# Optimization experiments

Measured on AMD Instinct MI355X. Metric: run time of the kernel, lower is better.

## Reference

```python
import jax, jax.numpy as jnp
import numpy as np

B, S, D, H, DFF = 2, 2048, 768, 12, 3072
DH = D // H
EPS = 1e-5


def _ln(x, g, b):
    m = jnp.mean(x, axis=-1, keepdims=True)
    v = jnp.mean((x - m) ** 2, axis=-1, keepdims=True)
    return (x - m) * jax.lax.rsqrt(v + EPS) * g + b


def setup_inputs() -> dict:
    key = jax.random.key(0)
    ks = jax.random.split(key, 13)
    sd = 1.0 / np.sqrt(D)
    sf = 1.0 / np.sqrt(DFF)
    return {
        "x": jax.random.normal(ks[0], (B, S, D), jnp.float32),
        "Wq": jax.random.uniform(ks[1], (D, D), jnp.float32, -sd, sd),
        "bq": jnp.zeros((D,), jnp.float32),
        "Wk": jax.random.uniform(ks[2], (D, D), jnp.float32, -sd, sd),
        "bk": jnp.zeros((D,), jnp.float32),
        "Wv": jax.random.uniform(ks[3], (D, D), jnp.float32, -sd, sd),
        "bv": jnp.zeros((D,), jnp.float32),
        "Wo": jax.random.uniform(ks[4], (D, D), jnp.float32, -sd, sd),
        "bo": jnp.zeros((D,), jnp.float32),
        "W1": jax.random.uniform(ks[5], (D, DFF), jnp.float32, -sd, sd),
        "b1": jnp.zeros((DFF,), jnp.float32),
        "W2": jax.random.uniform(ks[6], (DFF, D), jnp.float32, -sf, sf),
        "b2": jnp.zeros((D,), jnp.float32),
        "g1": jnp.ones((D,), jnp.float32),
        "be1": jnp.zeros((D,), jnp.float32),
        "g2": jnp.ones((D,), jnp.float32),
        "be2": jnp.zeros((D,), jnp.float32),
    }


def reference(x, Wq, bq, Wk, bk, Wv, bv, Wo, bo, W1, b1, W2, b2, g1, be1, g2, be2):
    # QKV projections, then split heads: [B,S,D] -> [B,H,S,DH]
    def heads(t):
        return t.reshape(B, S, H, DH).transpose(0, 2, 1, 3)
    Q = heads(x @ Wq + bq)
    K = heads(x @ Wk + bk)
    V = heads(x @ Wv + bv)
    # Per-head loop in original == batched-over-heads attention here (same math)
    scores = jnp.einsum("bhqd,bhkd->bhqk", Q, K) / np.sqrt(DH)
    attn = jax.nn.softmax(scores, axis=-1)  # [B,H,S,S] -- dominant intermediate
    ctx = jnp.einsum("bhqk,bhkd->bhqd", attn, V)
    ctx = ctx.transpose(0, 2, 1, 3).reshape(B, S, D)  # concat heads
    x = x + (ctx @ Wo + bo)
    x = _ln(x, g1, be1)
    ffn = (jax.nn.gelu(x @ W1 + b1, approximate=False)) @ W2 + b2
    x = _ln(x + ffn, g2, be2)
    return x
```

## Files before the change

kernel.cpp:

```cpp
#include <hip/hip_runtime.h>
#include <math.h>

#define BB 2
#define SS 2048
#define DD 768
#define HH 12
#define DHH 64
#define DFFN 3072
#define MTOK (BB*SS)

typedef __attribute__((ext_vector_type(8))) __bf16 bf16x8;
typedef __attribute__((ext_vector_type(4))) float f32x4;
typedef __attribute__((ext_vector_type(16))) float f32x16;

__device__ __forceinline__ unsigned short f2bf(float f) {
    unsigned int b = __builtin_bit_cast(unsigned int, f);
    b += 0x7FFFu + ((b >> 16) & 1u);
    return (unsigned short)(b >> 16);
}

__device__ __forceinline__ void gload_lds16(const void* g, void* l) {
    __builtin_amdgcn_global_load_lds((const __attribute__((address_space(1))) unsigned int*)g,
                                     (__attribute__((address_space(3))) unsigned int*)l,
                                     16, 0, 0);
}

template <int ACT, int OBF>
__global__ __launch_bounds__(256) void gemm_mfma(const unsigned short* __restrict__ A,
                                                 const unsigned short* __restrict__ Bt,
                                                 const float* __restrict__ bias,
                                                 void* __restrict__ Cout,
                                                 int M, int N, int ldA, int ldB, int Klen) {
    __shared__ unsigned short As[128 * 64];
    __shared__ unsigned short Bs[128 * 64];
    const int tid = threadIdx.x;
    const int lane = tid & 63;
    const int w = tid >> 6;
    const int l15 = lane & 15, l4 = lane >> 4;
    const int m0 = blockIdx.x * 128;
    const int n0 = blockIdx.y * 128;
    const int wr = (w >> 1) * 64;
    const int wc = (w & 1) * 64;

    f32x4 acc[4][4] = {};

    int srow[4], scd[4];
#pragma unroll
    for (int i = 0; i < 4; ++i) {
        int s = w * 256 + i * 64 + lane;
        srow[i] = s >> 3;
        scd[i] = (((s & 7) ^ (srow[i] & 7))) * 8;
    }

    for (int k0 = 0; k0 < Klen; k0 += 64) {
        __syncthreads();
#pragma unroll
        for (int i = 0; i < 4; ++i) {
            const unsigned short* gA = A + (size_t)(m0 + srow[i]) * ldA + k0 + scd[i];
            gload_lds16(gA, &As[(w * 256 + i * 64) * 8]);
        }
#pragma unroll
        for (int i = 0; i < 4; ++i) {
            const unsigned short* gB = Bt + (size_t)(n0 + srow[i]) * ldB + k0 + scd[i];
            gload_lds16(gB, &Bs[(w * 256 + i * 64) * 8]);
        }
        __syncthreads();
#pragma unroll
        for (int ks = 0; ks < 2; ++ks) {
            bf16x8 af[4], bfr[4];
#pragma unroll
            for (int m = 0; m < 4; ++m) {
                int r = wr + m * 16 + l15;
                int c = (ks * 4 + l4) ^ (r & 7);
                af[m] = *(const bf16x8*)&As[(r * 8 + c) * 8];
            }
#pragma unroll
            for (int n = 0; n < 4; ++n) {
                int r = wc + n * 16 + l15;
                int c = (ks * 4 + l4) ^ (r & 7);
                bfr[n] = *(const bf16x8*)&Bs[(r * 8 + c) * 8];
            }
#pragma unroll
            for (int m = 0; m < 4; ++m)
#pragma unroll
                for (int n = 0; n < 4; ++n)
                    acc[m][n] = __builtin_amdgcn_mfma_f32_16x16x32_bf16(af[m], bfr[n], acc[m][n], 0, 0, 0);
        }
    }

#pragma unroll
    for (int n = 0; n < 4; ++n) {
        int col = n0 + wc + n * 16 + l15;
        float bv = bias ? bias[col] : 0.0f;
#pragma unroll
        for (int m = 0; m < 4; ++m) {
#pragma unroll
            for (int r = 0; r < 4; ++r) {
                int row = m0 + wr + m * 16 + l4 * 4 + r;
                float v = acc[m][n][r] + bv;
                if (ACT) v = 0.5f * v * (1.0f + erff(v * 0.70710678118654752f));
                if (OBF) ((unsigned short*)Cout)[(size_t)row * N + col] = f2bf(v);
                else     ((float*)Cout)[(size_t)row * N + col] = v;
            }
        }
    }
}

__global__ __launch_bounds__(256) void attn_mfma2(const unsigned short* __restrict__ QKV,
                                                  const unsigned short* __restrict__ Vt,
                                                  unsigned short* __restrict__ Ctx) {
    __shared__ unsigned short Ks[64 * 64];
    __shared__ unsigned short Vs[64 * 64];
    const int tid = threadIdx.x;
    const int lane = tid & 63;
    const int w = tid >> 6;
    const int l31 = lane & 31;
    const int hi = lane >> 5;
    const int bh = blockIdx.y;
    const int b = bh / HH, h = bh % HH;
    const int q0 = blockIdx.x * 128 + w * 32;
    const float CLOG = 0.18033688011112042f;

    bf16x8 qf[4];
    {
        const unsigned short* qp = QKV + (size_t)(b * SS + q0 + l31) * 2304 + h * 64 + hi * 8;
        qf[0] = *(const bf16x8*)qp;
        qf[1] = *(const bf16x8*)(qp + 16);
        qf[2] = *(const bf16x8*)(qp + 32);
        qf[3] = *(const bf16x8*)(qp + 48);
    }

    f32x16 oacc[2] = {};
    float m_run = -1e30f, l_run = 0.0f;

    int arow[2], acd[2];
#pragma unroll
    for (int i = 0; i < 2; ++i) {
        int s = w * 128 + i * 64 + lane;
        arow[i] = s >> 3;
        acd[i] = ((s & 7) ^ (arow[i] & 7)) * 8;
    }

    for (int kt = 0; kt < SS / 64; ++kt) {
        const int k0 = kt * 64;
        __syncthreads();
#pragma unroll
        for (int i = 0; i < 2; ++i) {
            const unsigned short* gK = QKV + (size_t)(b * SS + k0 + arow[i]) * 2304 + DD + h * 64 + acd[i];
            gload_lds16(gK, &Ks[(w * 128 + i * 64) * 8]);
        }
#pragma unroll
        for (int i = 0; i < 2; ++i) {
            const unsigned short* gV = Vt + (size_t)(bh * 64 + arow[i]) * SS + k0 + acd[i];
            gload_lds16(gV, &Vs[(w * 128 + i * 64) * 8]);
        }
        __syncthreads();

        f32x16 st[2] = {};
#pragma unroll
        for (int t = 0; t < 2; ++t) {
#pragma unroll
            for (int ks = 0; ks < 4; ++ks) {
                int row = 32 * t + l31;
                int ch = (2 * ks + hi) ^ (row & 7);
                bf16x8 kf = *(const bf16x8*)&Ks[(row * 8 + ch) * 8];
                st[t] = __builtin_amdgcn_mfma_f32_32x32x16_bf16(kf, qf[ks], st[t], 0, 0, 0);
            }
        }

        float pmax = st[0][0];
#pragma unroll
        for (int r = 1; r < 16; ++r) pmax = fmaxf(pmax, st[0][r]);
#pragma unroll
        for (int r = 0; r < 16; ++r) pmax = fmaxf(pmax, st[1][r]);
        pmax = fmaxf(pmax, __shfl_xor(pmax, 32));
        pmax *= CLOG;
        const float mn = fmaxf(m_run, pmax);
        const float corr = exp2f(m_run - mn);

        unsigned int Wn[2][4][2];
        float rs = 0.0f;
#pragma unroll
        for (int t = 0; t < 2; ++t) {
#pragma unroll
            for (int blk = 0; blk < 4; ++blk) {
                float pa = exp2f(fmaf(st[t][4 * blk + 0], CLOG, -mn));
                float pb = exp2f(fmaf(st[t][4 * blk + 1], CLOG, -mn));
                float pc = exp2f(fmaf(st[t][4 * blk + 2], CLOG, -mn));
                float pd = exp2f(fmaf(st[t][4 * blk + 3], CLOG, -mn));
                rs += (pa + pb) + (pc + pd);
                Wn[t][blk][0] = (unsigned int)f2bf(pa) | ((unsigned int)f2bf(pb) << 16);
                Wn[t][blk][1] = (unsigned int)f2bf(pc) | ((unsigned int)f2bf(pd) << 16);
            }
        }
        rs += __shfl_xor(rs, 32);
        l_run = l_run * corr + rs;
        m_run = mn;

#pragma unroll
        for (int d = 0; d < 2; ++d)
#pragma unroll
            for (int r = 0; r < 16; ++r) oacc[d][r] *= corr;

        unsigned int PW[2][4][2];
#pragma unroll
        for (int t = 0; t < 2; ++t)
#pragma unroll
            for (int blk = 0; blk < 4; ++blk)
#pragma unroll
                for (int u = 0; u < 2; ++u) PW[t][blk][u] = __shfl_xor(Wn[t][blk][u], 32);

        const bool h1 = (hi == 1);
#pragma unroll
        for (int t = 0; t < 2; ++t) {
#pragma unroll
            for (int ks2 = 0; ks2 < 2; ++ks2) {
                union { unsigned int u[4]; bf16x8 v; } pu;
                pu.u[0] = h1 ? PW[t][2 * ks2 + 1][0] : Wn[t][2 * ks2][0];
                pu.u[1] = h1 ? PW[t][2 * ks2 + 1][1] : Wn[t][2 * ks2][1];
                pu.u[2] = h1 ? Wn[t][2 * ks2 + 1][0] : PW[t][2 * ks2][0];
                pu.u[3] = h1 ? Wn[t][2 * ks2 + 1][1] : PW[t][2 * ks2][1];
#pragma unroll
                for (int d = 0; d < 2; ++d) {
                    int row = 32 * d + l31;
                    int ch = (4 * t + 2 * ks2 + hi) ^ (row & 7);
                    bf16x8 vf = *(const bf16x8*)&Vs[(row * 8 + ch) * 8];
                    oacc[d] = __builtin_amdgcn_mfma_f32_32x32x16_bf16(vf, pu.v, oacc[d], 0, 0, 0);
                }
            }
        }
    }

    const float inv = 1.0f / l_run;
    unsigned short* cp = Ctx + (size_t)(b * SS + q0 + l31) * DD + h * 64;
#pragma unroll
    for (int d = 0; d < 2; ++d) {
#pragma unroll
        for (int blk = 0; blk < 4; ++blk) {
            unsigned long long pk =
                  (unsigned long long)f2bf(oacc[d][4 * blk + 0] * inv)
                | ((unsigned long long)f2bf(oacc[d][4 * blk + 1] * inv) << 16)
                | ((unsigned long long)f2bf(oacc[d][4 * blk + 2] * inv) << 32)
                | ((unsigned long long)f2bf(oacc[d][4 * blk + 3] * inv) << 48);
            *(unsigned long long*)(cp + 32 * d + 8 * blk + 4 * hi) = pk;
        }
    }
}

__global__ __launch_bounds__(256) void v_transpose(const unsigned short* __restrict__ QKV,
                                                   unsigned short* __restrict__ Vt) {
    __shared__ unsigned short t[64][66];
    const int tid = threadIdx.x;
    const int bh = blockIdx.y, b = bh / HH, h = bh % HH;
    const int s0 = blockIdx.x * 64;
    const int c = tid & 63, r0 = tid >> 6;
#pragma unroll
    for (int i = 0; i < 16; ++i) {
        int r = i * 4 + r0;
        t[r][c] = QKV[(size_t)(b * SS + s0 + r) * 2304 + 1536 + h * 64 + c];
    }
    __syncthreads();
#pragma unroll
    for (int i = 0; i < 16; ++i) {
        int r = i * 4 + r0;
        Vt[((size_t)bh * 64 + r) * SS + s0 + c] = t[c][r];
    }
}

__global__ __launch_bounds__(256) void wtrans(const float* __restrict__ W,
                                              unsigned short* __restrict__ Wt,
                                              int K, int N, int rowoff) {
    __shared__ float t[32][33];
    const int tid = threadIdx.x;
    const int k0 = blockIdx.x * 32, n0 = blockIdx.y * 32;
    const int c = tid & 31, r0 = tid >> 5;
#pragma unroll
    for (int i = 0; i < 4; ++i) {
        int r = i * 8 + r0;
        t[r][c] = W[(size_t)(k0 + r) * N + n0 + c];
    }
    __syncthreads();
#pragma unroll
    for (int i = 0; i < 4; ++i) {
        int r = i * 8 + r0;
        Wt[(size_t)(rowoff + n0 + r) * K + k0 + c] = f2bf(t[c][r]);
    }
}

__global__ __launch_bounds__(256) void f2b_vec(const float* __restrict__ in,
                                               unsigned short* __restrict__ out, int n4) {
    int i = blockIdx.x * 256 + threadIdx.x;
    if (i < n4) {
        float4 v = ((const float4*)in)[i];
        unsigned long long pk = (unsigned long long)f2bf(v.x)
                              | ((unsigned long long)f2bf(v.y) << 16)
                              | ((unsigned long long)f2bf(v.z) << 32)
                              | ((unsigned long long)f2bf(v.w) << 48);
        ((unsigned long long*)out)[i] = pk;
    }
}

__global__ __launch_bounds__(256) void bias_concat(const float* __restrict__ q,
                                                   const float* __restrict__ k,
                                                   const float* __restrict__ v,
                                                   float* __restrict__ o) {
    int i = blockIdx.x * 256 + threadIdx.x;
    if (i < DD) { o[i] = q[i]; o[DD + i] = k[i]; o[2 * DD + i] = v[i]; }
}

template <int WB>
__global__ __launch_bounds__(256) void add_ln3(const float* __restrict__ a,
                                               const float* __restrict__ p1,
                                               const float* __restrict__ p2,
                                               const float* __restrict__ bias,
                                               const float* __restrict__ g,
                                               const float* __restrict__ be,
                                               float* __restrict__ outf,
                                               unsigned short* __restrict__ outb) {
    const int row = blockIdx.x;
    const int tid = threadIdx.x;
    float x[3];
    float s = 0.0f, s2 = 0.0f;
#pragma unroll
    for (int i = 0; i < 3; ++i) {
        int c = tid + i * 256;
        size_t idx = (size_t)row * DD + c;
        float v = a[idx] + p1[idx] + p2[idx] + bias[c];
        x[i] = v; s += v; s2 += v * v;
    }
#pragma unroll
    for (int off = 32; off; off >>= 1) {
        s += __shfl_down(s, off);
        s2 += __shfl_down(s2, off);
    }
    __shared__ float ws[8];
    const int wid = tid >> 6, lane = tid & 63;
    if (lane == 0) { ws[wid] = s; ws[4 + wid] = s2; }
    __syncthreads();
    if (tid == 0) {
        ws[0] = ws[0] + ws[1] + ws[2] + ws[3];
        ws[4] = ws[4] + ws[5] + ws[6] + ws[7];
    }
    __syncthreads();
    const float mean = ws[0] * (1.0f / DD);
    const float var = ws[4] * (1.0f / DD) - mean * mean;
    const float inv = rsqrtf(var + 1e-5f);
#pragma unroll
    for (int i = 0; i < 3; ++i) {
        int c = tid + i * 256;
        float res = (x[i] - mean) * inv * g[c] + be[c];
        outf[(size_t)row * DD + c] = res;
        if (WB) outb[(size_t)row * DD + c] = f2bf(res);
    }
}

extern "C" void kernel_launch(void* const* d_in, const int* in_sizes, int n_in,
                              void* d_out, int out_size, void* d_ws, size_t ws_size,
                              hipStream_t stream) {
    const float* x   = (const float*)d_in[0];
    const float* Wq  = (const float*)d_in[1];
    const float* bq  = (const float*)d_in[2];
    const float* Wk  = (const float*)d_in[3];
    const float* bk  = (const float*)d_in[4];
    const float* Wv  = (const float*)d_in[5];
    const float* bv  = (const float*)d_in[6];
    const float* Wo  = (const float*)d_in[7];
    const float* bo  = (const float*)d_in[8];
    const float* W1  = (const float*)d_in[9];
    const float* b1  = (const float*)d_in[10];
    const float* W2  = (const float*)d_in[11];
    const float* b2  = (const float*)d_in[12];
    const float* g1  = (const float*)d_in[13];
    const float* be1 = (const float*)d_in[14];
    const float* g2  = (const float*)d_in[15];
    const float* be2 = (const float*)d_in[16];
    float* out = (float*)d_out;

    char* w8 = (char*)d_ws;
    unsigned short* QKV = (unsigned short*)w8;
    unsigned short* Hff = (unsigned short*)w8;
    unsigned short* Vt  = (unsigned short*)(w8 + 18874368);
    unsigned short* Ctxb  = (unsigned short*)(w8 + 25165824);
    unsigned short* xb    = (unsigned short*)(w8 + 31457280);
    unsigned short* Wqkvt = (unsigned short*)(w8 + 37748736);
    unsigned short* Wot   = (unsigned short*)(w8 + 41287680);
    unsigned short* W1t   = (unsigned short*)(w8 + 42467328);
    unsigned short* W2t   = (unsigned short*)(w8 + 47185920);
    float* bqkv = (float*)(w8 + 51904512);
    float* Pa   = (float*)(w8 + 51916800);
    float* Pb   = (float*)(w8 + 64499712);
    float* X2   = (float*)(w8 + 77082624);

    dim3 blk(256);

    f2b_vec<<<dim3(3072), blk, 0, stream>>>(x, xb, MTOK * DD / 4);
    wtrans<<<dim3(24, 24), blk, 0, stream>>>(Wq, Wqkvt, DD, DD, 0);
    wtrans<<<dim3(24, 24), blk, 0, stream>>>(Wk, Wqkvt, DD, DD, DD);
    wtrans<<<dim3(24, 24), blk, 0, stream>>>(Wv, Wqkvt, DD, DD, 2 * DD);
    wtrans<<<dim3(24, 24), blk, 0, stream>>>(Wo, Wot, DD, DD, 0);
    wtrans<<<dim3(24, 96), blk, 0, stream>>>(W1, W1t, DD, DFFN, 0);
    wtrans<<<dim3(96, 24), blk, 0, stream>>>(W2, W2t, DFFN, DD, 0);
    bias_concat<<<dim3(3), blk, 0, stream>>>(bq, bk, bv, bqkv);

    gemm_mfma<0, 1><<<dim3(32, 18), blk, 0, stream>>>(xb, Wqkvt, bqkv, QKV,
                                                      MTOK, 3 * DD, DD, DD, DD);
    v_transpose<<<dim3(32, 24), blk, 0, stream>>>(QKV, Vt);
    attn_mfma2<<<dim3(SS / 128, BB * HH), blk, 0, stream>>>(QKV, Vt, Ctxb);
    gemm_mfma<0, 0><<<dim3(32, 6), blk, 0, stream>>>(Ctxb, Wot, nullptr, Pa,
                                                     MTOK, DD, DD, DD, 384);
    gemm_mfma<0, 0><<<dim3(32, 6), blk, 0, stream>>>(Ctxb + 384, Wot + 384, nullptr, Pb,
                                                     MTOK, DD, DD, DD, 384);
    add_ln3<1><<<dim3(MTOK), blk, 0, stream>>>(x, Pa, Pb, bo, g1, be1, X2, xb);
    gemm_mfma<1, 1><<<dim3(32, 24), blk, 0, stream>>>(xb, W1t, b1, Hff,
                                                      MTOK, DFFN, DD, DD, DD);
    gemm_mfma<0, 0><<<dim3(32, 6), blk, 0, stream>>>(Hff, W2t, nullptr, Pa,
                                                     MTOK, DD, DFFN, DFFN, 1536);
    gemm_mfma<0, 0><<<dim3(32, 6), blk, 0, stream>>>(Hff + 1536, W2t + 1536, nullptr, Pb,
                                                     MTOK, DD, DFFN, DFFN, 1536);
    add_ln3<0><<<dim3(MTOK), blk, 0, stream>>>(X2, Pa, Pb, b2, g2, be2, out, nullptr);
}
```

Before: 387.2 us.

## Double-buffer GEMM/attention tiles, split attention KV in two, lazy softmax rescale

Adds double-buffered LDS prefetch to the GEMM and attention kernels so global loads overlap MFMA work. Attention is split across two KV halves via grid z, writing unnormalized float partials plus max/sum, merged by a new combine kernel. Online softmax skips rescaling unless the max grows by more than a threshold. Split-K GEMMs now use grid z instead of two launches. This adds partial-output traffic and an extra launch, and doubles LDS use per block.

```diff
diff --git a/kernel.cpp b/kernel.cpp
--- a/kernel.cpp
+++ b/kernel.cpp
@@ -31,16 +31,20 @@
                                                  const float* __restrict__ bias,
                                                  void* __restrict__ Cout,
                                                  int M, int N, int ldA, int ldB, int Klen) {
-    __shared__ unsigned short As[128 * 64];
-    __shared__ unsigned short Bs[128 * 64];
+    __shared__ unsigned short As[2 * 128 * 64];
+    __shared__ unsigned short Bs[2 * 128 * 64];
     const int tid = threadIdx.x;
     const int lane = tid & 63;
     const int w = tid >> 6;
     const int l15 = lane & 15, l4 = lane >> 4;
     const int m0 = blockIdx.x * 128;
     const int n0 = blockIdx.y * 128;
+    const int z = blockIdx.z;
     const int wr = (w >> 1) * 64;
     const int wc = (w & 1) * 64;
+
+    const unsigned short* Az = A + (size_t)z * Klen;
+    const unsigned short* Bz = Bt + (size_t)z * Klen;
 
     f32x4 acc[4][4] = {};
 
@@ -52,19 +56,27 @@
         scd[i] = (((s & 7) ^ (srow[i] & 7))) * 8;
     }
 
+#pragma unroll
+    for (int i = 0; i < 4; ++i) {
+        gload_lds16(Az + (size_t)(m0 + srow[i]) * ldA + scd[i], &As[(w * 256 + i * 64) * 8]);
+        gload_lds16(Bz + (size_t)(n0 + srow[i]) * ldB + scd[i], &Bs[(w * 256 + i * 64) * 8]);
+    }
+    __syncthreads();
+
+    int cb = 0;
     for (int k0 = 0; k0 < Klen; k0 += 64) {
-        __syncthreads();
-#pragma unroll
-        for (int i = 0; i < 4; ++i) {
-            const unsigned short* gA = A + (size_t)(m0 + srow[i]) * ldA + k0 + scd[i];
-            gload_lds16(gA, &As[(w * 256 + i * 64) * 8]);
-        }
-#pragma unroll
-        for (int i = 0; i < 4; ++i) {
-            const unsigned short* gB = Bt + (size_t)(n0 + srow[i]) * ldB + k0 + scd[i];
-            gload_lds16(gB, &Bs[(w * 256 + i * 64) * 8]);
-        }
-        __syncthreads();
+        if (k0 + 64 < Klen) {
+            const int nb = (cb ^ 1) * 128 * 64;
+#pragma unroll
+            for (int i = 0; i < 4; ++i) {
+                gload_lds16(Az + (size_t)(m0 + srow[i]) * ldA + k0 + 64 + scd[i],
+                            &As[nb + (w * 256 + i * 64) * 8]);
+                gload_lds16(Bz + (size_t)(n0 + srow[i]) * ldB + k0 + 64 + scd[i],
+                            &Bs[nb + (w * 256 + i * 64) * 8]);
+            }
+        }
+        const unsigned short* Ac = &As[cb * 128 * 64];
+        const unsigned short* Bc = &Bs[cb * 128 * 64];
 #pragma unroll
         for (int ks = 0; ks < 2; ++ks) {
             bf16x8 af[4], bfr[4];
@@ -72,13 +84,13 @@
             for (int m = 0; m < 4; ++m) {
                 int r = wr + m * 16 + l15;
                 int c = (ks * 4 + l4) ^ (r & 7);
-                af[m] = *(const bf16x8*)&As[(r * 8 + c) * 8];
+                af[m] = *(const bf16x8*)&Ac[(r * 8 + c) * 8];
             }
 #pragma unroll
             for (int n = 0; n < 4; ++n) {
                 int r = wc + n * 16 + l15;
                 int c = (ks * 4 + l4) ^ (r & 7);
-                bfr[n] = *(const bf16x8*)&Bs[(r * 8 + c) * 8];
+                bfr[n] = *(const bf16x8*)&Bc[(r * 8 + c) * 8];
             }
 #pragma unroll
             for (int m = 0; m < 4; ++m)
@@ -86,8 +98,11 @@
                 for (int n = 0; n < 4; ++n)
                     acc[m][n] = __builtin_amdgcn_mfma_f32_16x16x32_bf16(af[m], bfr[n], acc[m][n], 0, 0, 0);
         }
-    }
-
+        __syncthreads();
+        cb ^= 1;
+    }
+
+    const size_t zoff = (size_t)z * M * N;
 #pragma unroll
     for (int n = 0; n < 4; ++n) {
         int col = n0 + wc + n * 16 + l15;
@@ -100,17 +115,18 @@
                 float v = acc[m][n][r] + bv;
                 if (ACT) v = 0.5f * v * (1.0f + erff(v * 0.70710678118654752f));
                 if (OBF) ((unsigned short*)Cout)[(size_t)row * N + col] = f2bf(v);
-                else     ((float*)Cout)[(size_t)row * N + col] = v;
-            }
-        }
-    }
-}
-
-__global__ __launch_bounds__(256) void attn_mfma2(const unsigned short* __restrict__ QKV,
+                else     ((float*)Cout)[zoff + (size_t)row * N + col] = v;
+            }
+        }
+    }
+}
+
+__global__ __launch_bounds__(256) void attn_mfma3(const unsigned short* __restrict__ QKV,
                                                   const unsigned short* __restrict__ Vt,
-                                                  unsigned short* __restrict__ Ctx) {
-    __shared__ unsigned short Ks[64 * 64];
-    __shared__ unsigned short Vs[64 * 64];
+                                                  float* __restrict__ Opart,
+                                                  float* __restrict__ ML) {
+    __shared__ unsigned short Ks[2 * 64 * 64];
+    __shared__ unsigned short Vs[2 * 64 * 64];
     const int tid = threadIdx.x;
     const int lane = tid & 63;
     const int w = tid >> 6;
@@ -118,6 +134,7 @@
     const int hi = lane >> 5;
     const int bh = blockIdx.y;
     const int b = bh / HH, h = bh % HH;
+    const int z = blockIdx.z;
     const int q0 = blockIdx.x * 128 + w * 32;
     const float CLOG = 0.18033688011112042f;
 
@@ -141,20 +158,31 @@
         acd[i] = ((s & 7) ^ (arow[i] & 7)) * 8;
     }
 
-    for (int kt = 0; kt < SS / 64; ++kt) {
-        const int k0 = kt * 64;
-        __syncthreads();
-#pragma unroll
-        for (int i = 0; i < 2; ++i) {
-            const unsigned short* gK = QKV + (size_t)(b * SS + k0 + arow[i]) * 2304 + DD + h * 64 + acd[i];
-            gload_lds16(gK, &Ks[(w * 128 + i * 64) * 8]);
-        }
-#pragma unroll
-        for (int i = 0; i < 2; ++i) {
-            const unsigned short* gV = Vt + (size_t)(bh * 64 + arow[i]) * SS + k0 + acd[i];
-            gload_lds16(gV, &Vs[(w * 128 + i * 64) * 8]);
-        }
-        __syncthreads();
+    const int kbase = z * (SS / 2);
+#pragma unroll
+    for (int i = 0; i < 2; ++i) {
+        gload_lds16(QKV + (size_t)(b * SS + kbase + arow[i]) * 2304 + DD + h * 64 + acd[i],
+                    &Ks[(w * 128 + i * 64) * 8]);
+        gload_lds16(Vt + (size_t)(bh * 64 + arow[i]) * SS + kbase + acd[i],
+                    &Vs[(w * 128 + i * 64) * 8]);
+    }
+    __syncthreads();
+
+    int cb = 0;
+    for (int it = 0; it < SS / 128; ++it) {
+        if (it + 1 < SS / 128) {
+            const int k0n = kbase + (it + 1) * 64;
+            const int nb = (cb ^ 1) * 64 * 64;
+#pragma unroll
+            for (int i = 0; i < 2; ++i) {
+                gload_lds16(QKV + (size_t)(b * SS + k0n + arow[i]) * 2304 + DD + h * 64 + acd[i],
+                            &Ks[nb + (w * 128 + i * 64) * 8]);
+                gload_lds16(Vt + (size_t)(bh * 64 + arow[i]) * SS + k0n + acd[i],
+                            &Vs[nb + (w * 128 + i * 64) * 8]);
+            }
+        }
+        const unsigned short* Kc = &Ks[cb * 64 * 64];
+        const unsigned short* Vc = &Vs[cb * 64 * 64];
 
         f32x16 st[2] = {};
 #pragma unroll
@@ -163,7 +191,7 @@
             for (int ks = 0; ks < 4; ++ks) {
                 int row = 32 * t + l31;
                 int ch = (2 * ks + hi) ^ (row & 7);
-                bf16x8 kf = *(const bf16x8*)&Ks[(row * 8 + ch) * 8];
+                bf16x8 kf = *(const bf16x8*)&Kc[(row * 8 + ch) * 8];
                 st[t] = __builtin_amdgcn_mfma_f32_32x32x16_bf16(kf, qf[ks], st[t], 0, 0, 0);
             }
         }
@@ -175,8 +203,17 @@
         for (int r = 0; r < 16; ++r) pmax = fmaxf(pmax, st[1][r]);
         pmax = fmaxf(pmax, __shfl_xor(pmax, 32));
         pmax *= CLOG;
-        const float mn = fmaxf(m_run, pmax);
-        const float corr = exp2f(m_run - mn);
+
+        if (!__all(pmax <= m_run + 8.0f)) {
+            float mn = fmaxf(m_run, pmax);
+            float corr = exp2f(m_run - mn);
+#pragma unroll
+            for (int d = 0; d < 2; ++d)
+#pragma unroll
+                for (int r = 0; r < 16; ++r) oacc[d][r] *= corr;
+            l_run *= corr;
+            m_run = mn;
+        }
 
         unsigned int Wn[2][4][2];
         float rs = 0.0f;
@@ -184,66 +221,80 @@
         for (int t = 0; t < 2; ++t) {
 #pragma unroll
             for (int blk = 0; blk < 4; ++blk) {
-                float pa = exp2f(fmaf(st[t][4 * blk + 0], CLOG, -mn));
-                float pb = exp2f(fmaf(st[t][4 * blk + 1], CLOG, -mn));
-                float pc = exp2f(fmaf(st[t][4 * blk + 2], CLOG, -mn));
-                float pd = exp2f(fmaf(st[t][4 * blk + 3], CLOG, -mn));
+                float pa = exp2f(fmaf(st[t][4 * blk + 0], CLOG, -m_run));
+                float pb = exp2f(fmaf(st[t][4 * blk + 1], CLOG, -m_run));
+                float pc = exp2f(fmaf(st[t][4 * blk + 2], CLOG, -m_run));
+                float pd = exp2f(fmaf(st[t][4 * blk + 3], CLOG, -m_run));
                 rs += (pa + pb) + (pc + pd);
                 Wn[t][blk][0] = (unsigned int)f2bf(pa) | ((unsigned int)f2bf(pb) << 16);
                 Wn[t][blk][1] = (unsigned int)f2bf(pc) | ((unsigned int)f2bf(pd) << 16);
             }
         }
         rs += __shfl_xor(rs, 32);
-        l_run = l_run * corr + rs;
-        m_run = mn;
-
-#pragma unroll
-        for (int d = 0; d < 2; ++d)
-#pragma unroll
-            for (int r = 0; r < 16; ++r) oacc[d][r] *= corr;
-
-        unsigned int PW[2][4][2];
-#pragma unroll
-        for (int t = 0; t < 2; ++t)
-#pragma unroll
-            for (int blk = 0; blk < 4; ++blk)
-#pragma unroll
-                for (int u = 0; u < 2; ++u) PW[t][blk][u] = __shfl_xor(Wn[t][blk][u], 32);
-
-        const bool h1 = (hi == 1);
+        l_run += rs;
+
 #pragma unroll
         for (int t = 0; t < 2; ++t) {
 #pragma unroll
             for (int ks2 = 0; ks2 < 2; ++ks2) {
+                unsigned int ex0 = __shfl_xor(hi ? Wn[t][2 * ks2][0] : Wn[t][2 * ks2 + 1][0], 32);
+                unsigned int ex1 = __shfl_xor(hi ? Wn[t][2 * ks2][1] : Wn[t][2 * ks2 + 1][1], 32);
                 union { unsigned int u[4]; bf16x8 v; } pu;
-                pu.u[0] = h1 ? PW[t][2 * ks2 + 1][0] : Wn[t][2 * ks2][0];
-                pu.u[1] = h1 ? PW[t][2 * ks2 + 1][1] : Wn[t][2 * ks2][1];
-                pu.u[2] = h1 ? Wn[t][2 * ks2 + 1][0] : PW[t][2 * ks2][0];
-                pu.u[3] = h1 ? Wn[t][2 * ks2 + 1][1] : PW[t][2 * ks2][1];
+                pu.u[0] = hi ? ex0 : Wn[t][2 * ks2][0];
+                pu.u[1] = hi ? ex1 : Wn[t][2 * ks2][1];
+                pu.u[2] = hi ? Wn[t][2 * ks2 + 1][0] : ex0;
+                pu.u[3] = hi ? Wn[t][2 * ks2 + 1][1] : ex1;
 #pragma unroll
                 for (int d = 0; d < 2; ++d) {
                     int row = 32 * d + l31;
                     int ch = (4 * t + 2 * ks2 + hi) ^ (row & 7);
-                    bf16x8 vf = *(const bf16x8*)&Vs[(row * 8 + ch) * 8];
+                    bf16x8 vf = *(const bf16x8*)&Vc[(row * 8 + ch) * 8];
                     oacc[d] = __builtin_amdgcn_mfma_f32_32x32x16_bf16(vf, pu.v, oacc[d], 0, 0, 0);
                 }
             }
         }
-    }
-
-    const float inv = 1.0f / l_run;
-    unsigned short* cp = Ctx + (size_t)(b * SS + q0 + l31) * DD + h * 64;
+        __syncthreads();
+        cb ^= 1;
+    }
+
+    float* op = Opart + (size_t)z * MTOK * DD + (size_t)(b * SS + q0 + l31) * DD + h * 64;
 #pragma unroll
     for (int d = 0; d < 2; ++d) {
 #pragma unroll
         for (int blk = 0; blk < 4; ++blk) {
-            unsigned long long pk =
-                  (unsigned long long)f2bf(oacc[d][4 * blk + 0] * inv)
-                | ((unsigned long long)f2bf(oacc[d][4 * blk + 1] * inv) << 16)
-                | ((unsigned long long)f2bf(oacc[d][4 * blk + 2] * inv) << 32)
-                | ((unsigned long long)f2bf(oacc[d][4 * blk + 3] * inv) << 48);
-            *(unsigned long long*)(cp + 32 * d + 8 * blk + 4 * hi) = pk;
-        }
+            float4 v = make_float4(oacc[d][4 * blk + 0], oacc[d][4 * blk + 1],
+                                   oacc[d][4 * blk + 2], oacc[d][4 * blk + 3]);
+            *(float4*)(op + 32 * d + 8 * blk + 4 * hi) = v;
+        }
+    }
+    if (hi == 0) {
+        size_t mi = (((size_t)z * BB * HH + bh) * SS + (q0 + l31)) * 2;
+        ML[mi] = m_run;
+        ML[mi + 1] = l_run;
+    }
+}
+
+__global__ __launch_bounds__(256) void attn_combine(const float* __restrict__ Opart,
+                                                    const float* __restrict__ ML,
+                                                    unsigned short* __restrict__ Ctx) {
+    const int row = blockIdx.x;
+    const int tid = threadIdx.x;
+    const int b = row >> 11, s = row & 2047;
+    const float* r0 = Opart + (size_t)row * DD;
+    const float* r1 = Opart + (size_t)MTOK * DD + (size_t)row * DD;
+    unsigned short* co = Ctx + (size_t)row * DD;
+#pragma unroll
+    for (int i = 0; i < 3; ++i) {
+        int c = tid + i * 256;
+        int h = c >> 6;
+        size_t i0 = (((size_t)(b * HH + h)) * SS + s) * 2;
+        size_t i1 = (((size_t)(BB * HH + b * HH + h)) * SS + s) * 2;
+        float m0 = ML[i0], l0 = ML[i0 + 1];
+        float m1 = ML[i1], l1 = ML[i1 + 1];
+        float M = fmaxf(m0, m1);
+        float w0 = exp2f(m0 - M), w1 = exp2f(m1 - M);
+        float inv = 1.0f / (w0 * l0 + w1 * l1);
+        co[c] = f2bf((r0[c] * w0 + r1[c] * w1) * inv);
     }
 }
 
@@ -390,6 +441,7 @@
     float* Pa   = (float*)(w8 + 51916800);
     float* Pb   = (float*)(w8 + 64499712);
     float* X2   = (float*)(w8 + 77082624);
+    float* ML   = (float*)(w8 + 89665536);
 
     dim3 blk(256);
 
@@ -402,20 +454,17 @@
     wtrans<<<dim3(96, 24), blk, 0, stream>>>(W2, W2t, DFFN, DD, 0);
     bias_concat<<<dim3(3), blk, 0, stream>>>(bq, bk, bv, bqkv);
 
-    gemm_mfma<0, 1><<<dim3(32, 18), blk, 0, stream>>>(xb, Wqkvt, bqkv, QKV,
-                                                      MTOK, 3 * DD, DD, DD, DD);
+    gemm_mfma<0, 1><<<dim3(32, 18, 1), blk, 0, stream>>>(xb, Wqkvt, bqkv, QKV,
+                                                         MTOK, 3 * DD, DD, DD, DD);
     v_transpose<<<dim3(32, 24), blk, 0, stream>>>(QKV, Vt);
-    attn_mfma2<<<dim3(SS / 128, BB * HH), blk, 0, stream>>>(QKV, Vt, Ctxb);
-    gemm_mfma<0, 0><<<dim3(32, 6), blk, 0, stream>>>(Ctxb, Wot, nullptr, Pa,
-                                                     MTOK, DD, DD, DD, 384);
-    gemm_mfma<0, 0><<<dim3(32, 6), blk, 0, stream>>>(Ctxb + 384, Wot + 384, nullptr, Pb,
-                                                     MTOK, DD, DD, DD, 384);
+    attn_mfma3<<<dim3(SS / 128, BB * HH, 2), blk, 0, stream>>>(QKV, Vt, Pa, ML);
+    attn_combine<<<dim3(MTOK), blk, 0, stream>>>(Pa, ML, Ctxb);
+    gemm_mfma<0, 0><<<dim3(32, 6, 2), blk, 0, stream>>>(Ctxb, Wot, nullptr, Pa,
+                                                        MTOK, DD, DD, DD, 384);
     add_ln3<1><<<dim3(MTOK), blk, 0, stream>>>(x, Pa, Pb, bo, g1, be1, X2, xb);
-    gemm_mfma<1, 1><<<dim3(32, 24), blk, 0, stream>>>(xb, W1t, b1, Hff,
-                                                      MTOK, DFFN, DD, DD, DD);
-    gemm_mfma<0, 0><<<dim3(32, 6), blk, 0, stream>>>(Hff, W2t, nullptr, Pa,
-                                                     MTOK, DD, DFFN, DFFN, 1536);
-    gemm_mfma<0, 0><<<dim3(32, 6), blk, 0, stream>>>(Hff + 1536, W2t + 1536, nullptr, Pb,
-                                                     MTOK, DD, DFFN, DFFN, 1536);
+    gemm_mfma<1, 1><<<dim3(32, 24, 1), blk, 0, stream>>>(xb, W1t, b1, Hff,
+                                                         MTOK, DFFN, DD, DD, DD);
+    gemm_mfma<0, 0><<<dim3(32, 6, 2), blk, 0, stream>>>(Hff, W2t, nullptr, Pa,
+                                                        MTOK, DD, DFFN, DFFN, 1536);
     add_ln3<0><<<dim3(MTOK), blk, 0, stream>>>(X2, Pa, Pb, b2, g2, be2, out, nullptr);
 }
```

Result: faster. 345.7 us (-10.7%).
